# Kernel tuning notes

Measured on AMD Instinct MI355X. Metric: run time of the kernel, lower is better.

## Reference

```python
import jax, jax.numpy as jnp
import numpy as np

B, T, D = 4, 2048, 1024
H, HS = 16, 64  # num heads, head size; H*HS == D


def setup_inputs() -> dict:
    key = jax.random.key(0)
    ks = jax.random.split(key, 6)
    scale = D ** -0.5
    x = jax.random.normal(ks[0], (B, T, D), dtype=jnp.float32)
    # per-head projections, stacked: [H, D, HS]
    Wq = jax.random.normal(ks[1], (H, D, HS), dtype=jnp.float32) * scale
    Wk = jax.random.normal(ks[2], (H, D, HS), dtype=jnp.float32) * scale
    Wv = jax.random.normal(ks[3], (H, D, HS), dtype=jnp.float32) * scale
    # output projection: [H*HS, D] + bias [D]
    Wp = jax.random.normal(ks[4], (H * HS, D), dtype=jnp.float32) * ((H * HS) ** -0.5)
    bp = jax.random.normal(ks[5], (D,), dtype=jnp.float32) * 0.01
    return {"x": x, "Wq": Wq, "Wk": Wk, "Wv": Wv, "Wp": Wp, "bp": bp}


def reference(x, Wq, Wk, Wv, Wp, bp):
    # per-head Q, K, V projections (batched over heads): [B, H, T, HS]
    q = jnp.einsum('btd,hde->bhte', x, Wq)
    k = jnp.einsum('btd,hde->bhte', x, Wk)
    v = jnp.einsum('btd,hde->bhte', x, Wv)
    # scaled scores with causal mask: [B, H, T, T]
    scores = jnp.einsum('bhte,bhse->bhts', q, k) * (HS ** -0.5)
    causal = jnp.tril(jnp.ones((T, T), dtype=bool))
    scores = jnp.where(causal, scores, jnp.float32(-jnp.inf))
    wei = jax.nn.softmax(scores, axis=-1)  # dropout is identity at eval
    out = jnp.einsum('bhts,bhse->bhte', wei, v)
    # concat heads -> [B, T, H*HS], then output projection
    out = out.transpose(0, 2, 1, 3).reshape(B, T, H * HS)
    return out @ Wp + bp
```

## Files before the change

### kernel.cpp

```cpp
#include <hip/hip_runtime.h>
#include <stdint.h>

typedef __attribute__((ext_vector_type(8))) short short8;
typedef __attribute__((ext_vector_type(4))) float f32x4;
typedef __attribute__((ext_vector_type(16))) float f32x16;

__device__ __forceinline__ unsigned short f2bf(float f) {
  unsigned u = __float_as_uint(f);
  u = u + 0x7FFFu + ((u >> 16) & 1u);
  return (unsigned short)(u >> 16);
}
__device__ __forceinline__ unsigned cvtpk_bf16(float lo, float hi) {
  unsigned r;
  asm("v_cvt_pk_bf16_f32 %0, %1, %2" : "=v"(r) : "v"(lo), "v"(hi));
  return r;
}
__device__ __forceinline__ float fast_exp2(float x) {
#if __has_builtin(__builtin_amdgcn_exp2f)
  return __builtin_amdgcn_exp2f(x);
#else
  return exp2f(x);
#endif
}
__device__ __forceinline__ void gl2lds16(const void* g, void* l) {
  __builtin_amdgcn_global_load_lds(
      (const __attribute__((address_space(1))) void*)(uintptr_t)g,
      (__attribute__((address_space(3))) void*)(uintptr_t)l, 16, 0, 0);
}

__global__ __launch_bounds__(256) void pack_all_kernel(const float* __restrict__ x,
                                                       const float* __restrict__ Wq,
                                                       const float* __restrict__ Wk,
                                                       const float* __restrict__ Wv,
                                                       const float* __restrict__ Wp,
                                                       ushort* __restrict__ xb,
                                                       ushort* __restrict__ WqkvT,
                                                       ushort* __restrict__ WpT) {
  __shared__ float tile[64][65];
  const int bid0 = blockIdx.x;
  const int tid = threadIdx.x;
  if (bid0 < 4096) {
    int i = (bid0 * 256 + tid) * 8;
    float4 a = *(const float4*)(x + i);
    float4 b = *(const float4*)(x + i + 4);
    uint4 o;
    o.x = (unsigned)f2bf(a.x) | ((unsigned)f2bf(a.y) << 16);
    o.y = (unsigned)f2bf(a.z) | ((unsigned)f2bf(a.w) << 16);
    o.z = (unsigned)f2bf(b.x) | ((unsigned)f2bf(b.y) << 16);
    o.w = (unsigned)f2bf(b.z) | ((unsigned)f2bf(b.w) << 16);
    *(uint4*)(xb + i) = o;
    return;
  }
  const int bid = bid0 - 4096;
  const int lr = tid >> 6;
  const int lc = tid & 63;
  if (bid < 768) {
    const int s = bid >> 8;
    const int rem = bid & 255;
    const int h = rem >> 4;
    const int dt = rem & 15;
    const float* W = (s == 0) ? Wq : (s == 1) ? Wk : Wv;
    const float scale = (s == 0) ? 0.18033688011f : 1.0f;
#pragma unroll
    for (int p = 0; p < 16; ++p) {
      int r = p * 4 + lr;
      tile[r][lc] = W[(size_t)(h * 1024 + dt * 64 + r) * 64 + lc];
    }
    __syncthreads();
#pragma unroll
    for (int p = 0; p < 16; ++p) {
      int e = p * 4 + lr;
      float v = tile[lc][e] * scale;
      WqkvT[(size_t)(s * 1024 + h * 64 + e) * 1024 + dt * 64 + lc] = f2bf(v);
    }
  } else {
    const int t = bid - 768;
    const int rt = t >> 4, ct = t & 15;
#pragma unroll
    for (int p = 0; p < 16; ++p) {
      int r = p * 4 + lr;
      tile[r][lc] = Wp[(size_t)(rt * 64 + r) * 1024 + ct * 64 + lc];
    }
    __syncthreads();
#pragma unroll
    for (int p = 0; p < 16; ++p) {
      int c = p * 4 + lr;
      float v = tile[lc][c];
      WpT[(size_t)(ct * 64 + c) * 1024 + rt * 64 + lc] = f2bf(v);
    }
  }
}

template <int OUT_MODE>
__global__ __launch_bounds__(256) void gemm_bt(const ushort* __restrict__ A,
                                               const ushort* __restrict__ BT,
                                               ushort* __restrict__ Cb,
                                               float* __restrict__ Cf,
                                               const float* __restrict__ bias,
                                               int M, int N, int K) {
  __shared__ __align__(16) ushort Al[128 * 64];
  __shared__ __align__(16) ushort Bl[128 * 64];
  const int tid = threadIdx.x;
  const int lane = tid & 63;
  const int wave = tid >> 6;
  const int wm = wave >> 1, wn = wave & 1;
  const int nbx = gridDim.x;
  const int nwg = nbx * gridDim.y;
  int wg = blockIdx.y * nbx + blockIdx.x;
  wg = (wg & 7) * (nwg >> 3) + (wg >> 3);
  const int m0 = (wg / nbx) * 128, n0 = (wg % nbx) * 128;
  const int r16 = lane & 15, g = lane >> 4;
  f32x4 acc[4][4] = {};
  const int kTiles = K >> 6;
  const size_t ldb = (size_t)K * 2;
  const int srow = tid >> 3;
  const int scol = ((tid & 7) * 16) ^ (((tid >> 3) & 7) << 4);
  const char* a_src = (const char*)A + (size_t)(m0 + srow) * ldb + scol;
  const char* b_src = (const char*)BT + (size_t)(n0 + srow) * ldb + scol;
  char* a_d = (char*)Al + wave * 1024;
  char* b_d = (char*)Bl + wave * 1024;
  const size_t row32 = (size_t)32 * ldb;
  for (int kt = 0; kt < kTiles; ++kt) {
    const size_t k0b = (size_t)kt * 128;
    if (kt) __syncthreads();
#pragma unroll
    for (int i = 0; i < 4; ++i) {
      gl2lds16(a_src + i * row32 + k0b, a_d + i * 4096);
      gl2lds16(b_src + i * row32 + k0b, b_d + i * 4096);
    }
    __syncthreads();
    short8 af[4][2], bf2[4][2];
#pragma unroll
    for (int i = 0; i < 4; ++i) {
      const int ra = (wm * 64 + i * 16 + r16) * 128;
      const int rb = (wn * 64 + i * 16 + r16) * 128;
      const int sw = (r16 & 7) << 4;
#pragma unroll
      for (int ks = 0; ks < 2; ++ks) {
        af[i][ks] = *(const short8*)((const char*)Al + ra + ((ks * 64 + g * 16) ^ sw));
        bf2[i][ks] = *(const short8*)((const char*)Bl + rb + ((ks * 64 + g * 16) ^ sw));
      }
    }
#pragma unroll
    for (int ks = 0; ks < 2; ++ks)
#pragma unroll
      for (int mi = 0; mi < 4; ++mi)
#pragma unroll
        for (int ni = 0; ni < 4; ++ni)
          acc[mi][ni] = __builtin_amdgcn_mfma_f32_16x16x32_bf16(af[mi][ks], bf2[ni][ks],
                                                                acc[mi][ni], 0, 0, 0);
  }
#pragma unroll
  for (int mi = 0; mi < 4; ++mi)
#pragma unroll
    for (int ni = 0; ni < 4; ++ni)
#pragma unroll
      for (int r = 0; r < 4; ++r) {
        int row = m0 + wm * 64 + mi * 16 + g * 4 + r;
        int col = n0 + wn * 64 + ni * 16 + r16;
        float v = acc[mi][ni][r];
        if (OUT_MODE == 0) {
          Cb[(size_t)row * N + col] = f2bf(v);
        } else {
          Cf[(size_t)row * N + col] = v + bias[col];
        }
      }
}

__global__ __launch_bounds__(256) void attn_mfma_kernel(const ushort* __restrict__ QKV,
                                                        ushort* __restrict__ O) {
  int flat = blockIdx.z * 128 + blockIdx.y * 8 + blockIdx.x;
  flat = (flat & 7) * 64 + (flat >> 3);
  const int qtA = flat & 7;
  const int h = (flat >> 3) & 15;
  const int b = flat >> 7;
  __shared__ __align__(16) ushort Kl[2][64 * 64];
  __shared__ __align__(16) ushort VT[64 * 64];
  const int tid = threadIdx.x;
  const int lane = tid & 63;
  const int wave = tid >> 6;
  const int lo5 = lane & 31;
  const int hi = lane >> 5;

  short8 ones;
#pragma unroll
  for (int i = 0; i < 8; ++i) ones[i] = (short)0x3F80;

  const int k_key0 = wave * 16 + (lane >> 3);
  const int k_key1 = k_key0 + 8;
  const int ksrc_off0 = ((lane & 7) * 16) ^ ((k_key0 & 7) << 4);
  const int ksrc_off1 = ((lane & 7) * 16) ^ ((k_key1 & 7) << 4);
  const char* kgbase = (const char*)(QKV + ((size_t)b * 2048) * 3072 + 1024 + h * 64);
  const int kp2 = (tid & 31) * 2;
  const int dg = tid >> 5;
  const char* vgbase = (const char*)(QKV + ((size_t)b * 2048) * 3072 + 2048 + h * 64 + dg * 8);

#pragma unroll
  for (int ph = 0; ph < 2; ++ph) {
    const int qt = ph ? qtA : (15 - qtA);
    const int qbase = qt * 128 + wave * 32;
    const int qg = qbase + lo5;

    short8 qf[4];
    {
      const ushort* qp = QKV + ((size_t)(b * 2048 + qbase + lo5) * 3072) + h * 64 + hi * 8;
#pragma unroll
      for (int dc = 0; dc < 4; ++dc) qf[dc] = *(const short8*)(qp + dc * 16);
    }

    f32x16 o0 = {}, o1 = {}, lacc = {};
    const int nblk = qt * 2 + 2;

    uint4 nv0, nv1;
    {
      const char* vp = vgbase + (size_t)kp2 * 6144;
      nv0 = *(const uint4*)(vp);
      nv1 = *(const uint4*)(vp + 6144);
    }
    __syncthreads();
    gl2lds16(kgbase + (size_t)k_key0 * 6144 + ksrc_off0, (char*)Kl[0] + wave * 2048);
    gl2lds16(kgbase + (size_t)k_key1 * 6144 + ksrc_off1, (char*)Kl[0] + wave * 2048 + 1024);

    int cur = 0;
    for (int blk = 0; blk < nblk; ++blk) {
      const int s0 = blk * 64;
      __syncthreads();
      {
        const ushort* e0 = (const ushort*)&nv0;
        const ushort* e1 = (const ushort*)&nv1;
#pragma unroll
        for (int j = 0; j < 8; ++j) {
          const int row = dg * 8 + j;
          *(unsigned*)((char*)VT + row * 128 + ((kp2 * 2) ^ ((row & 7) << 4))) =
              (unsigned)e0[j] | ((unsigned)e1[j] << 16);
        }
      }
      __syncthreads();

      if (blk + 1 < nblk) {
        char* kd = (char*)Kl[cur ^ 1] + wave * 2048;
        gl2lds16(kgbase + (size_t)(s0 + 64 + k_key0) * 6144 + ksrc_off0, kd);
        gl2lds16(kgbase + (size_t)(s0 + 64 + k_key1) * 6144 + ksrc_off1, kd + 1024);
        const char* vp = vgbase + (size_t)(s0 + 64 + kp2) * 6144;
        nv0 = *(const uint4*)(vp);
        nv1 = *(const uint4*)(vp + 6144);
      }

      const ushort* Kb = Kl[cur];
#pragma unroll
      for (int g2 = 0; g2 < 2; ++g2) {
        const int ks = s0 + g2 * 32;
        if (ks > qbase + 31) continue;
        f32x16 s_acc = {};
        const int krow = g2 * 32 + lo5;
        const char* ksrc = (const char*)Kb + krow * 128;
        const int ksw = (krow & 7) << 4;
#pragma unroll
        for (int dc = 0; dc < 4; ++dc) {
          short8 kf = *(const short8*)(ksrc + ((dc * 32 + hi * 16) ^ ksw));
          s_acc = __builtin_amdgcn_mfma_f32_32x32x16_bf16(kf, qf[dc], s_acc, 0, 0, 0);
        }
        float p[16];
        if (ks + 31 > qbase) {
          const int ksg = ks + 4 * hi;
#pragma unroll
          for (int r = 0; r < 16; ++r) {
            const int key_g = ksg + (r & 3) + 8 * (r >> 2);
            float pv = fast_exp2(s_acc[r]);
            p[r] = (key_g <= qg) ? pv : 0.f;
          }
        } else {
#pragma unroll
          for (int r = 0; r < 16; ++r) p[r] = fast_exp2(s_acc[r]);
        }
#pragma unroll
        for (int kc = 0; kc < 2; ++kc) {
          unsigned w0 = cvtpk_bf16(p[kc * 8 + 0], p[kc * 8 + 1]);
          unsigned w2 = cvtpk_bf16(p[kc * 8 + 4], p[kc * 8 + 5]);
          unsigned w1 = cvtpk_bf16(p[kc * 8 + 2], p[kc * 8 + 3]);
          unsigned w3 = cvtpk_bf16(p[kc * 8 + 6], p[kc * 8 + 7]);
          asm("v_permlane32_swap_b32 %0, %1" : "+v"(w0), "+v"(w2));
          asm("v_permlane32_swap_b32 %0, %1" : "+v"(w1), "+v"(w3));
          uint4 paw;
          paw.x = w0; paw.y = w1; paw.z = w2; paw.w = w3;
          short8 pa = *(short8*)&paw;
          const int kb = (g2 * 32 + kc * 16 + hi * 8) * 2;
          lacc = __builtin_amdgcn_mfma_f32_32x32x16_bf16(pa, ones, lacc, 0, 0, 0);
          {
            const int vrow = lo5;
            short8 vf =
                *(const short8*)((const char*)VT + vrow * 128 + (kb ^ ((vrow & 7) << 4)));
            o0 = __builtin_amdgcn_mfma_f32_32x32x16_bf16(pa, vf, o0, 0, 0, 0);
          }
          {
            const int vrow = 32 + lo5;
            short8 vf =
                *(const short8*)((const char*)VT + vrow * 128 + (kb ^ ((vrow & 7) << 4)));
            o1 = __builtin_amdgcn_mfma_f32_32x32x16_bf16(pa, vf, o1, 0, 0, 0);
          }
        }
      }
      cur ^= 1;
    }

#pragma unroll
    for (int r = 0; r < 16; ++r) {
      const int qr = (r & 3) + 8 * (r >> 2) + 4 * hi;
      const float li = 1.f / lacc[r];
      ushort* ob = O + ((size_t)(b * 2048 + qbase + qr) * 1024) + h * 64 + lo5;
      ob[0] = f2bf(o0[r] * li);
      ob[32] = f2bf(o1[r] * li);
    }
  }
}

extern "C" void kernel_launch(void* const* d_in, const int* in_sizes, int n_in,
                              void* d_out, int out_size, void* d_ws, size_t ws_size,
                              hipStream_t stream) {
  const float* x = (const float*)d_in[0];
  const float* Wq = (const float*)d_in[1];
  const float* Wk = (const float*)d_in[2];
  const float* Wv = (const float*)d_in[3];
  const float* Wp = (const float*)d_in[4];
  const float* bp = (const float*)d_in[5];
  float* out = (float*)d_out;

  ushort* xb = (ushort*)d_ws;
  ushort* WqkvT = xb + 8388608;
  ushort* WpT = WqkvT + 3145728;
  ushort* QKV = WpT + 1048576;
  ushort* O = QKV + 25165824;

  pack_all_kernel<<<5120, 256, 0, stream>>>(x, Wq, Wk, Wv, Wp, xb, WqkvT, WpT);
  gemm_bt<0><<<dim3(24, 64), 256, 0, stream>>>(xb, WqkvT, QKV, nullptr, nullptr,
                                               8192, 3072, 1024);
  attn_mfma_kernel<<<dim3(8, 16, 4), 256, 0, stream>>>(QKV, O);
  gemm_bt<1><<<dim3(8, 64), 256, 0, stream>>>(O, WpT, nullptr, out, bp,
                                              8192, 1024, 1024);
}
```

Measured before the change: 154.6 us.

## Run both paired causal query tiles concurrently with 8 waves per block

The attention kernel used to process its two paired query tiles (qt and 15-qt) one after the other with 4 waves. It now launches 512 threads, with waves 0-3 handling the long tile and waves 4-7 the short one at the same time. The two tiles share the K/V LDS staging over 32-2*qtA blocks, and the per-thread load work is halved. The aim is more waves in flight to hide latency and to remove the second phase's reloads. In exchange, waves on the short tile sit idle at barriers while the long tile's extra blocks run, and register pressure at 512 threads may limit occupancy.

```diff
diff --git a/kernel.cpp b/kernel.cpp
--- a/kernel.cpp
+++ b/kernel.cpp
@@ -167,7 +167,7 @@
       }
 }
 
-__global__ __launch_bounds__(256) void attn_mfma_kernel(const ushort* __restrict__ QKV,
+__global__ __launch_bounds__(512) void attn_mfma_kernel(const ushort* __restrict__ QKV,
                                                         ushort* __restrict__ O) {
   int flat = blockIdx.z * 128 + blockIdx.y * 8 + blockIdx.x;
   flat = (flat & 7) * 64 + (flat >> 3);
@@ -181,136 +181,128 @@
   const int wave = tid >> 6;
   const int lo5 = lane & 31;
   const int hi = lane >> 5;
+  const int qt = (wave >> 2) ? qtA : (15 - qtA);
+  const int qbase = qt * 128 + (wave & 3) * 32;
+  const int qg = qbase + lo5;
 
   short8 ones;
 #pragma unroll
   for (int i = 0; i < 8; ++i) ones[i] = (short)0x3F80;
 
-  const int k_key0 = wave * 16 + (lane >> 3);
-  const int k_key1 = k_key0 + 8;
-  const int ksrc_off0 = ((lane & 7) * 16) ^ ((k_key0 & 7) << 4);
-  const int ksrc_off1 = ((lane & 7) * 16) ^ ((k_key1 & 7) << 4);
+  const int k_key = wave * 8 + (lane >> 3);
+  const int ksrc_off = ((lane & 7) * 16) ^ ((k_key & 7) << 4);
   const char* kgbase = (const char*)(QKV + ((size_t)b * 2048) * 3072 + 1024 + h * 64);
   const int kp2 = (tid & 31) * 2;
   const int dg = tid >> 5;
-  const char* vgbase = (const char*)(QKV + ((size_t)b * 2048) * 3072 + 2048 + h * 64 + dg * 8);
-
-#pragma unroll
-  for (int ph = 0; ph < 2; ++ph) {
-    const int qt = ph ? qtA : (15 - qtA);
-    const int qbase = qt * 128 + wave * 32;
-    const int qg = qbase + lo5;
-
-    short8 qf[4];
+  const char* vgbase =
+      (const char*)(QKV + ((size_t)b * 2048) * 3072 + 2048 + h * 64 + dg * 4);
+
+  short8 qf[4];
+  {
+    const ushort* qp = QKV + ((size_t)(b * 2048 + qbase + lo5) * 3072) + h * 64 + hi * 8;
+#pragma unroll
+    for (int dc = 0; dc < 4; ++dc) qf[dc] = *(const short8*)(qp + dc * 16);
+  }
+
+  f32x16 o0 = {}, o1 = {}, lacc = {};
+  const int nblk = 32 - 2 * qtA;
+
+  uint2 nv0, nv1;
+  {
+    const char* vp = vgbase + (size_t)kp2 * 6144;
+    nv0 = *(const uint2*)vp;
+    nv1 = *(const uint2*)(vp + 6144);
+  }
+  gl2lds16(kgbase + (size_t)k_key * 6144 + ksrc_off, (char*)Kl[0] + wave * 1024);
+
+  int cur = 0;
+  for (int blk = 0; blk < nblk; ++blk) {
+    const int s0 = blk * 64;
+    __syncthreads();
     {
-      const ushort* qp = QKV + ((size_t)(b * 2048 + qbase + lo5) * 3072) + h * 64 + hi * 8;
-#pragma unroll
-      for (int dc = 0; dc < 4; ++dc) qf[dc] = *(const short8*)(qp + dc * 16);
-    }
-
-    f32x16 o0 = {}, o1 = {}, lacc = {};
-    const int nblk = qt * 2 + 2;
-
-    uint4 nv0, nv1;
-    {
-      const char* vp = vgbase + (size_t)kp2 * 6144;
-      nv0 = *(const uint4*)(vp);
-      nv1 = *(const uint4*)(vp + 6144);
-    }
-    __syncthreads();
-    gl2lds16(kgbase + (size_t)k_key0 * 6144 + ksrc_off0, (char*)Kl[0] + wave * 2048);
-    gl2lds16(kgbase + (size_t)k_key1 * 6144 + ksrc_off1, (char*)Kl[0] + wave * 2048 + 1024);
-
-    int cur = 0;
-    for (int blk = 0; blk < nblk; ++blk) {
-      const int s0 = blk * 64;
-      __syncthreads();
-      {
-        const ushort* e0 = (const ushort*)&nv0;
-        const ushort* e1 = (const ushort*)&nv1;
-#pragma unroll
-        for (int j = 0; j < 8; ++j) {
-          const int row = dg * 8 + j;
-          *(unsigned*)((char*)VT + row * 128 + ((kp2 * 2) ^ ((row & 7) << 4))) =
-              (unsigned)e0[j] | ((unsigned)e1[j] << 16);
+      const ushort* e0 = (const ushort*)&nv0;
+      const ushort* e1 = (const ushort*)&nv1;
+#pragma unroll
+      for (int j = 0; j < 4; ++j) {
+        const int row = dg * 4 + j;
+        *(unsigned*)((char*)VT + row * 128 + ((kp2 * 2) ^ ((row & 7) << 4))) =
+            (unsigned)e0[j] | ((unsigned)e1[j] << 16);
+      }
+    }
+    __syncthreads();
+
+    if (blk + 1 < nblk) {
+      gl2lds16(kgbase + (size_t)(s0 + 64 + k_key) * 6144 + ksrc_off,
+               (char*)Kl[cur ^ 1] + wave * 1024);
+      const char* vp = vgbase + (size_t)(s0 + 64 + kp2) * 6144;
+      nv0 = *(const uint2*)vp;
+      nv1 = *(const uint2*)(vp + 6144);
+    }
+
+    const ushort* Kb = Kl[cur];
+#pragma unroll
+    for (int g2 = 0; g2 < 2; ++g2) {
+      const int ks = s0 + g2 * 32;
+      if (ks > qbase + 31) continue;
+      f32x16 s_acc = {};
+      const int krow = g2 * 32 + lo5;
+      const char* ksrc = (const char*)Kb + krow * 128;
+      const int ksw = (krow & 7) << 4;
+#pragma unroll
+      for (int dc = 0; dc < 4; ++dc) {
+        short8 kf = *(const short8*)(ksrc + ((dc * 32 + hi * 16) ^ ksw));
+        s_acc = __builtin_amdgcn_mfma_f32_32x32x16_bf16(kf, qf[dc], s_acc, 0, 0, 0);
+      }
+      float p[16];
+      if (ks + 31 > qbase) {
+        const int ksg = ks + 4 * hi;
+#pragma unroll
+        for (int r = 0; r < 16; ++r) {
+          const int key_g = ksg + (r & 3) + 8 * (r >> 2);
+          float pv = fast_exp2(s_acc[r]);
+          p[r] = (key_g <= qg) ? pv : 0.f;
         }
-      }
-      __syncthreads();
-
-      if (blk + 1 < nblk) {
-        char* kd = (char*)Kl[cur ^ 1] + wave * 2048;
-        gl2lds16(kgbase + (size_t)(s0 + 64 + k_key0) * 6144 + ksrc_off0, kd);
-        gl2lds16(kgbase + (size_t)(s0 + 64 + k_key1) * 6144 + ksrc_off1, kd + 1024);
-        const char* vp = vgbase + (size_t)(s0 + 64 + kp2) * 6144;
-        nv0 = *(const uint4*)(vp);
-        nv1 = *(const uint4*)(vp + 6144);
-      }
-
-      const ushort* Kb = Kl[cur];
-#pragma unroll
-      for (int g2 = 0; g2 < 2; ++g2) {
-        const int ks = s0 + g2 * 32;
-        if (ks > qbase + 31) continue;
-        f32x16 s_acc = {};
-        const int krow = g2 * 32 + lo5;
-        const char* ksrc = (const char*)Kb + krow * 128;
-        const int ksw = (krow & 7) << 4;
-#pragma unroll
-        for (int dc = 0; dc < 4; ++dc) {
-          short8 kf = *(const short8*)(ksrc + ((dc * 32 + hi * 16) ^ ksw));
-          s_acc = __builtin_amdgcn_mfma_f32_32x32x16_bf16(kf, qf[dc], s_acc, 0, 0, 0);
+      } else {
+#pragma unroll
+        for (int r = 0; r < 16; ++r) p[r] = fast_exp2(s_acc[r]);
+      }
+#pragma unroll
+      for (int kc = 0; kc < 2; ++kc) {
+        unsigned w0 = cvtpk_bf16(p[kc * 8 + 0], p[kc * 8 + 1]);
+        unsigned w2 = cvtpk_bf16(p[kc * 8 + 4], p[kc * 8 + 5]);
+        unsigned w1 = cvtpk_bf16(p[kc * 8 + 2], p[kc * 8 + 3]);
+        unsigned w3 = cvtpk_bf16(p[kc * 8 + 6], p[kc * 8 + 7]);
+        asm("v_permlane32_swap_b32 %0, %1" : "+v"(w0), "+v"(w2));
+        asm("v_permlane32_swap_b32 %0, %1" : "+v"(w1), "+v"(w3));
+        uint4 paw;
+        paw.x = w0; paw.y = w1; paw.z = w2; paw.w = w3;
+        short8 pa = *(short8*)&paw;
+        const int kb = (g2 * 32 + kc * 16 + hi * 8) * 2;
+        lacc = __builtin_amdgcn_mfma_f32_32x32x16_bf16(pa, ones, lacc, 0, 0, 0);
+        {
+          const int vrow = lo5;
+          short8 vf =
+              *(const short8*)((const char*)VT + vrow * 128 + (kb ^ ((vrow & 7) << 4)));
+          o0 = __builtin_amdgcn_mfma_f32_32x32x16_bf16(pa, vf, o0, 0, 0, 0);
         }
-        float p[16];
-        if (ks + 31 > qbase) {
-          const int ksg = ks + 4 * hi;
-#pragma unroll
-          for (int r = 0; r < 16; ++r) {
-            const int key_g = ksg + (r & 3) + 8 * (r >> 2);
-            float pv = fast_exp2(s_acc[r]);
-            p[r] = (key_g <= qg) ? pv : 0.f;
-          }
-        } else {
-#pragma unroll
-          for (int r = 0; r < 16; ++r) p[r] = fast_exp2(s_acc[r]);
+        {
+          const int vrow = 32 + lo5;
+          short8 vf =
+              *(const short8*)((const char*)VT + vrow * 128 + (kb ^ ((vrow & 7) << 4)));
+          o1 = __builtin_amdgcn_mfma_f32_32x32x16_bf16(pa, vf, o1, 0, 0, 0);
         }
-#pragma unroll
-        for (int kc = 0; kc < 2; ++kc) {
-          unsigned w0 = cvtpk_bf16(p[kc * 8 + 0], p[kc * 8 + 1]);
-          unsigned w2 = cvtpk_bf16(p[kc * 8 + 4], p[kc * 8 + 5]);
-          unsigned w1 = cvtpk_bf16(p[kc * 8 + 2], p[kc * 8 + 3]);
-          unsigned w3 = cvtpk_bf16(p[kc * 8 + 6], p[kc * 8 + 7]);
-          asm("v_permlane32_swap_b32 %0, %1" : "+v"(w0), "+v"(w2));
-          asm("v_permlane32_swap_b32 %0, %1" : "+v"(w1), "+v"(w3));
-          uint4 paw;
-          paw.x = w0; paw.y = w1; paw.z = w2; paw.w = w3;
-          short8 pa = *(short8*)&paw;
-          const int kb = (g2 * 32 + kc * 16 + hi * 8) * 2;
-          lacc = __builtin_amdgcn_mfma_f32_32x32x16_bf16(pa, ones, lacc, 0, 0, 0);
-          {
-            const int vrow = lo5;
-            short8 vf =
-                *(const short8*)((const char*)VT + vrow * 128 + (kb ^ ((vrow & 7) << 4)));
-            o0 = __builtin_amdgcn_mfma_f32_32x32x16_bf16(pa, vf, o0, 0, 0, 0);
-          }
-          {
-            const int vrow = 32 + lo5;
-            short8 vf =
-                *(const short8*)((const char*)VT + vrow * 128 + (kb ^ ((vrow & 7) << 4)));
-            o1 = __builtin_amdgcn_mfma_f32_32x32x16_bf16(pa, vf, o1, 0, 0, 0);
-          }
-        }
-      }
-      cur ^= 1;
-    }
-
-#pragma unroll
-    for (int r = 0; r < 16; ++r) {
-      const int qr = (r & 3) + 8 * (r >> 2) + 4 * hi;
-      const float li = 1.f / lacc[r];
-      ushort* ob = O + ((size_t)(b * 2048 + qbase + qr) * 1024) + h * 64 + lo5;
-      ob[0] = f2bf(o0[r] * li);
-      ob[32] = f2bf(o1[r] * li);
-    }
+      }
+    }
+    cur ^= 1;
+  }
+
+#pragma unroll
+  for (int r = 0; r < 16; ++r) {
+    const int qr = (r & 3) + 8 * (r >> 2) + 4 * hi;
+    const float li = 1.f / lacc[r];
+    ushort* ob = O + ((size_t)(b * 2048 + qbase + qr) * 1024) + h * 64 + lo5;
+    ob[0] = f2bf(o0[r] * li);
+    ob[32] = f2bf(o1[r] * li);
   }
 }
 
@@ -334,7 +326,7 @@
   pack_all_kernel<<<5120, 256, 0, stream>>>(x, Wq, Wk, Wv, Wp, xb, WqkvT, WpT);
   gemm_bt<0><<<dim3(24, 64), 256, 0, stream>>>(xb, WqkvT, QKV, nullptr, nullptr,
                                                8192, 3072, 1024);
-  attn_mfma_kernel<<<dim3(8, 16, 4), 256, 0, stream>>>(QKV, O);
+  attn_mfma_kernel<<<dim3(8, 16, 4), 512, 0, stream>>>(QKV, O);
   gemm_bt<1><<<dim3(8, 64), 256, 0, stream>>>(O, WpT, nullptr, out, bp,
                                               8192, 1024, 1024);
 }
```

After: 166.8 us. +7.9%, slower.

## Split attention key range across two blocks and merge partials in a combine kernel

Applied to the files above, without the earlier changes.

Each (batch, head, query-tile) attention block is now split into two blocks that process alternating 64-key blocks. Each block writes unnormalized bf16 partial outputs and per-row softmax denominators, reusing scratch buffers that are no longer needed (xb and the packed-weight region). A new combine kernel adds the two partials and divides by the summed denominators. This doubles the attention grid to raise parallelism and occupancy, at the cost of an extra memory-bound pass and bf16 rounding of unnormalized partial sums.

```diff
diff --git a/kernel.cpp b/kernel.cpp
--- a/kernel.cpp
+++ b/kernel.cpp
@@ -168,12 +168,16 @@
 }
 
 __global__ __launch_bounds__(256) void attn_mfma_kernel(const ushort* __restrict__ QKV,
-                                                        ushort* __restrict__ O) {
-  int flat = blockIdx.z * 128 + blockIdx.y * 8 + blockIdx.x;
-  flat = (flat & 7) * 64 + (flat >> 3);
+                                                        ushort* __restrict__ O0,
+                                                        ushort* __restrict__ O1,
+                                                        float* __restrict__ Lbuf) {
+  int flat = blockIdx.z * 256 + blockIdx.y * 16 + blockIdx.x;
+  flat = (flat & 7) * 128 + (flat >> 3);
   const int qtA = flat & 7;
-  const int h = (flat >> 3) & 15;
-  const int b = flat >> 7;
+  const int sp = (flat >> 3) & 1;
+  const int h = (flat >> 4) & 15;
+  const int b = flat >> 8;
+  ushort* Opart = sp ? O1 : O0;
   __shared__ __align__(16) ushort Kl[2][64 * 64];
   __shared__ __align__(16) ushort VT[64 * 64];
   const int tid = threadIdx.x;
@@ -213,16 +217,18 @@
 
     uint4 nv0, nv1;
     {
-      const char* vp = vgbase + (size_t)kp2 * 6144;
+      const char* vp = vgbase + (size_t)(sp * 64 + kp2) * 6144;
       nv0 = *(const uint4*)(vp);
       nv1 = *(const uint4*)(vp + 6144);
     }
     __syncthreads();
-    gl2lds16(kgbase + (size_t)k_key0 * 6144 + ksrc_off0, (char*)Kl[0] + wave * 2048);
-    gl2lds16(kgbase + (size_t)k_key1 * 6144 + ksrc_off1, (char*)Kl[0] + wave * 2048 + 1024);
+    gl2lds16(kgbase + (size_t)(sp * 64 + k_key0) * 6144 + ksrc_off0,
+             (char*)Kl[0] + wave * 2048);
+    gl2lds16(kgbase + (size_t)(sp * 64 + k_key1) * 6144 + ksrc_off1,
+             (char*)Kl[0] + wave * 2048 + 1024);
 
     int cur = 0;
-    for (int blk = 0; blk < nblk; ++blk) {
+    for (int blk = sp; blk < nblk; blk += 2) {
       const int s0 = blk * 64;
       __syncthreads();
       {
@@ -237,11 +243,11 @@
       }
       __syncthreads();
 
-      if (blk + 1 < nblk) {
+      if (blk + 2 < nblk) {
         char* kd = (char*)Kl[cur ^ 1] + wave * 2048;
-        gl2lds16(kgbase + (size_t)(s0 + 64 + k_key0) * 6144 + ksrc_off0, kd);
-        gl2lds16(kgbase + (size_t)(s0 + 64 + k_key1) * 6144 + ksrc_off1, kd + 1024);
-        const char* vp = vgbase + (size_t)(s0 + 64 + kp2) * 6144;
+        gl2lds16(kgbase + (size_t)(s0 + 128 + k_key0) * 6144 + ksrc_off0, kd);
+        gl2lds16(kgbase + (size_t)(s0 + 128 + k_key1) * 6144 + ksrc_off1, kd + 1024);
+        const char* vp = vgbase + (size_t)(s0 + 128 + kp2) * 6144;
         nv0 = *(const uint4*)(vp);
         nv1 = *(const uint4*)(vp + 6144);
       }
@@ -306,12 +312,37 @@
 #pragma unroll
     for (int r = 0; r < 16; ++r) {
       const int qr = (r & 3) + 8 * (r >> 2) + 4 * hi;
-      const float li = 1.f / lacc[r];
-      ushort* ob = O + ((size_t)(b * 2048 + qbase + qr) * 1024) + h * 64 + lo5;
-      ob[0] = f2bf(o0[r] * li);
-      ob[32] = f2bf(o1[r] * li);
-    }
-  }
+      const int grow = b * 2048 + qbase + qr;
+      ushort* ob = Opart + ((size_t)grow * 1024) + h * 64 + lo5;
+      ob[0] = f2bf(o0[r]);
+      ob[32] = f2bf(o1[r]);
+      if (lo5 == 0) Lbuf[sp * 131072 + grow * 16 + h] = lacc[r];
+    }
+  }
+}
+
+__global__ __launch_bounds__(256) void combine_kernel(const ushort* __restrict__ P1,
+                                                      const float* __restrict__ L,
+                                                      ushort* __restrict__ O) {
+  const int idx = (blockIdx.x * 256 + threadIdx.x) * 8;
+  const int row = idx >> 10;
+  const int hh = (idx >> 6) & 15;
+  const float inv = 1.f / (L[row * 16 + hh] + L[131072 + row * 16 + hh]);
+  uint4 a = *(const uint4*)(O + idx);
+  uint4 b = *(const uint4*)(P1 + idx);
+  const unsigned* au = (const unsigned*)&a;
+  const unsigned* bu = (const unsigned*)&b;
+  uint4 o;
+  unsigned* ou = (unsigned*)&o;
+#pragma unroll
+  for (int i = 0; i < 4; ++i) {
+    float a0 = __uint_as_float(au[i] << 16);
+    float a1 = __uint_as_float(au[i] & 0xFFFF0000u);
+    float b0 = __uint_as_float(bu[i] << 16);
+    float b1 = __uint_as_float(bu[i] & 0xFFFF0000u);
+    ou[i] = (unsigned)f2bf((a0 + b0) * inv) | ((unsigned)f2bf((a1 + b1) * inv) << 16);
+  }
+  *(uint4*)(O + idx) = o;
 }
 
 extern "C" void kernel_launch(void* const* d_in, const int* in_sizes, int n_in,
@@ -330,11 +361,13 @@
   ushort* WpT = WqkvT + 3145728;
   ushort* QKV = WpT + 1048576;
   ushort* O = QKV + 25165824;
+  float* Lbuf = (float*)WqkvT;
 
   pack_all_kernel<<<5120, 256, 0, stream>>>(x, Wq, Wk, Wv, Wp, xb, WqkvT, WpT);
   gemm_bt<0><<<dim3(24, 64), 256, 0, stream>>>(xb, WqkvT, QKV, nullptr, nullptr,
                                                8192, 3072, 1024);
-  attn_mfma_kernel<<<dim3(8, 16, 4), 256, 0, stream>>>(QKV, O);
+  attn_mfma_kernel<<<dim3(16, 16, 4), 256, 0, stream>>>(QKV, O, xb, Lbuf);
+  combine_kernel<<<4096, 256, 0, stream>>>(xb, Lbuf, O);
   gemm_bt<1><<<dim3(8, 64), 256, 0, stream>>>(O, WpT, nullptr, out, bp,
                                               8192, 1024, 1024);
 }
```

Result: slower. 168.0 us (+8.6%).
